# Optimization experiments

Hardware: AMD Instinct MI355X
Metric: run time of the kernel (lower is better)

Reference implementation:

```python
import jax, jax.numpy as jnp
import numpy as np

B, T_IN, D = 8, 512, 384
N_FORMANTS = 1
MAX_DUR = 8               # durations drawn in [0, 8)
T_MEL = T_IN * (MAX_DUR - 1)  # 3584, upper bound on sum of durations
MEL_MAX_LEN = 2048        # static mel_max_len clamp (regulate_len's mel_max_len path)
PACE = 1.0


def setup_inputs() -> dict:
    key = jax.random.key(0)
    k1, k2, k3 = jax.random.split(key, 3)
    enc_out = jax.random.normal(k1, (B, T_IN, D), jnp.float32)
    durations = jax.random.randint(k2, (B, T_IN), 0, MAX_DUR)
    pitch = jax.random.normal(k3, (B, N_FORMANTS, T_MEL), jnp.float32)
    return {"enc_out": enc_out, "durations": durations, "pitch": pitch}


def _regulate_len(durations, enc_out, pace, mel_max_len):
    # reps = round(dur / pace) via floor(x + 0.5), matching torch (reps + 0.5).long()
    reps = jnp.floor(durations.astype(jnp.float32) / pace + 0.5).astype(jnp.int32)  # [B, T_in]
    dec_lens = jnp.minimum(reps.sum(axis=1), mel_max_len)                           # [B]
    # exclusive/inclusive cumsum boundaries, cast to enc dtype as in torch
    cums = jnp.cumsum(jnp.pad(reps, ((0, 0), (1, 0))), axis=1).astype(enc_out.dtype)  # [B, T_in+1]
    rng = jnp.arange(mel_max_len, dtype=enc_out.dtype)[None, :, None]                 # [1, M, 1]
    # one-hot expansion matrix: frame m belongs to token t iff cums[t] <= m < cums[t+1]
    mult = ((cums[:, None, :-1] <= rng) & (cums[:, None, 1:] > rng)).astype(enc_out.dtype)  # [B, M, T_in]
    enc_rep = jnp.einsum('bmt,btd->bmd', mult, enc_out)                               # [B, M, D]
    return enc_rep, dec_lens


def _average_pitch(pitch, durs):
    # pitch: [B, F, T_mel], durs: [B, T_in] (frame counts per token)
    ends = jnp.cumsum(durs, axis=1)                      # [B, T_in] inclusive ends
    starts = jnp.pad(ends[:, :-1], ((0, 0), (1, 0)))     # [B, T_in] exclusive starts
    pc = jnp.pad(jnp.cumsum(pitch, axis=2), ((0, 0), (0, 0), (1, 0)))                         # [B, F, T_mel+1]
    pnz = jnp.pad(jnp.cumsum((pitch != 0.0).astype(pitch.dtype), axis=2), ((0, 0), (0, 0), (1, 0)))
    nf = pitch.shape[1]
    dce = jnp.broadcast_to(ends[:, None, :], (ends.shape[0], nf, ends.shape[1]))
    dcs = jnp.broadcast_to(starts[:, None, :], dce.shape)
    sums = jnp.take_along_axis(pc, dce, axis=2) - jnp.take_along_axis(pc, dcs, axis=2)
    nelems = jnp.take_along_axis(pnz, dce, axis=2) - jnp.take_along_axis(pnz, dcs, axis=2)
    safe = jnp.where(nelems == 0.0, 1.0, nelems)
    return jnp.where(nelems == 0.0, 0.0, sums / safe)   # [B, F, T_in]


def reference(enc_out, durations, pitch):
    enc_rep, dec_lens = _regulate_len(durations, enc_out, PACE, MEL_MAX_LEN)
    pitch_avg = _average_pitch(pitch, durations)
    return enc_rep, dec_lens, pitch_avg
```

## Files before the change

kernel.cpp:

```cpp
#include <hip/hip_runtime.h>

typedef float floatx4 __attribute__((ext_vector_type(4)));

#define NB 8
#define T_IN 512
#define D 384
#define D4 96
#define T_MEL 3584
#define MEL_MAX 2048

#define FRAMES_PER_BLOCK 16
#define GB_PER_BATCH (MEL_MAX / FRAMES_PER_BLOCK)
#define GATHER_BLOCKS (NB * GB_PER_BATCH)
#define PITCH_BLOCKS  (NB * 2)

#define DEC_OFF  ((size_t)NB * MEL_MAX * D)
#define PITCH_OFF (DEC_OFF + NB)

__global__ __launch_bounds__(256) void fp_fused_kernel(
    const int* __restrict__ dur,
    const floatx4* __restrict__ enc4,
    const float* __restrict__ pitch,
    float* __restrict__ out)
{
    const int bid = blockIdx.x;
    const int tid = threadIdx.x;
    const bool isPitch = bid >= GATHER_BLOCKS;
    const int b = isPitch ? ((bid - GATHER_BLOCKS) >> 1) : (bid / GB_PER_BATCH);

    __shared__ int s_ends[T_IN];
    __shared__ int s_wsum[4];
    __shared__ int s_map[FRAMES_PER_BLOCK];

    const int2 dd = ((const int2*)(dur + b * T_IN))[tid];
    int x = dd.x + dd.y;
    #pragma unroll
    for (int off = 1; off < 64; off <<= 1) {
        int y = __shfl_up(x, off, 64);
        if ((tid & 63) >= off) x += y;
    }
    if ((tid & 63) == 63) s_wsum[tid >> 6] = x;
    __syncthreads();
    int woff = 0, total = 0;
    #pragma unroll
    for (int i = 0; i < 4; ++i) {
        int v = s_wsum[i];
        if (i < (tid >> 6)) woff += v;
        total += v;
    }
    const int e1 = woff + x;
    s_ends[2 * tid]     = e1 - dd.y;
    s_ends[2 * tid + 1] = e1;
    __syncthreads();

    if (!isPitch) {
        const int f0 = (bid % GB_PER_BATCH) * FRAMES_PER_BLOCK;
        if (tid < FRAMES_PER_BLOCK) {
            const int f = f0 + tid;
            int tok = -1;
            if (f < total) {
                int lo = 0, hi = T_IN;
                while (lo < hi) {
                    int mid = (lo + hi) >> 1;
                    if (s_ends[mid] > f) hi = mid; else lo = mid + 1;
                }
                tok = lo;
            }
            s_map[tid] = tok;
        }
        if (tid == 0 && bid == b * GB_PER_BATCH)
            out[DEC_OFF + b] = (float)(total < MEL_MAX ? total : MEL_MAX);
        __syncthreads();

        const floatx4* erow = enc4 + (size_t)b * T_IN * D4;
        floatx4* orow = (floatx4*)out + ((size_t)b * MEL_MAX + f0) * D4;
        #pragma unroll
        for (int it = 0; it < (FRAMES_PER_BLOCK * D4) / 256; ++it) {
            const int idx = it * 256 + tid;
            const int fl  = idx / D4;
            const int d4  = idx - fl * D4;
            const int tok = s_map[fl];
            floatx4 v = (floatx4)(0.0f);
            if (tok >= 0) v = erow[(size_t)tok * D4 + d4];
            orow[idx] = v;
        }
    } else {
        const int half = (bid - GATHER_BLOCKS) & 1;
        const int tk = half * 256 + tid;
        const int end   = s_ends[tk];
        const int start = tk ? s_ends[tk - 1] : 0;
        const float* p = pitch + (size_t)b * T_MEL;
        float acc = 0.0f;
        int cnt = 0;
        for (int m = start; m < end; ++m) {
            float v = p[m];
            acc += v;
            cnt += (v != 0.0f) ? 1 : 0;
        }
        out[PITCH_OFF + b * T_IN + tk] = cnt ? acc / (float)cnt : 0.0f;
    }
}

extern "C" void kernel_launch(void* const* d_in, const int* in_sizes, int n_in,
                              void* d_out, int out_size, void* d_ws, size_t ws_size,
                              hipStream_t stream) {
    const float* enc   = (const float*)d_in[0];
    const int*   dur   = (const int*)d_in[1];
    const float* pitch = (const float*)d_in[2];
    float* out = (float*)d_out;

    fp_fused_kernel<<<GATHER_BLOCKS + PITCH_BLOCKS, 256, 0, stream>>>(
        dur, (const floatx4*)enc, pitch, out);
}
```

Measured before the change: 11.83 us.

## Scatter token indices into frame map instead of binary search over shared ends

Drops the shared s_ends array and its extra barrier. Each thread now writes its two tokens' frame ranges directly into the per-block frame-to-token map, replacing a per-frame binary search done by only 16 threads. The pitch path uses one block per batch, with each thread averaging two tokens and storing a float2, and the dec_lens write moves to the pitch blocks. This cuts prologue latency per block, but the scatter loops are serial per thread and the pitch blocks now each do twice the serial work.

```diff
diff --git a/kernel.cpp b/kernel.cpp
--- a/kernel.cpp
+++ b/kernel.cpp
@@ -12,7 +12,7 @@
 #define FRAMES_PER_BLOCK 16
 #define GB_PER_BATCH (MEL_MAX / FRAMES_PER_BLOCK)
 #define GATHER_BLOCKS (NB * GB_PER_BATCH)
-#define PITCH_BLOCKS  (NB * 2)
+#define PITCH_BLOCKS  NB
 
 #define DEC_OFF  ((size_t)NB * MEL_MAX * D)
 #define PITCH_OFF (DEC_OFF + NB)
@@ -26,11 +26,12 @@
     const int bid = blockIdx.x;
     const int tid = threadIdx.x;
     const bool isPitch = bid >= GATHER_BLOCKS;
-    const int b = isPitch ? ((bid - GATHER_BLOCKS) >> 1) : (bid / GB_PER_BATCH);
+    const int b = isPitch ? (bid - GATHER_BLOCKS) : (bid >> 7);
 
-    __shared__ int s_ends[T_IN];
     __shared__ int s_wsum[4];
     __shared__ int s_map[FRAMES_PER_BLOCK];
+
+    if (!isPitch && tid < FRAMES_PER_BLOCK) s_map[tid] = -1;
 
     const int2 dd = ((const int2*)(dur + b * T_IN))[tid];
     int x = dd.x + dd.y;
@@ -48,28 +49,21 @@
         if (i < (tid >> 6)) woff += v;
         total += v;
     }
-    const int e1 = woff + x;
-    s_ends[2 * tid]     = e1 - dd.y;
-    s_ends[2 * tid + 1] = e1;
-    __syncthreads();
+    const int end1   = woff + x;
+    const int start1 = end1 - dd.y;
+    const int start0 = start1 - dd.x;
 
     if (!isPitch) {
-        const int f0 = (bid % GB_PER_BATCH) * FRAMES_PER_BLOCK;
-        if (tid < FRAMES_PER_BLOCK) {
-            const int f = f0 + tid;
-            int tok = -1;
-            if (f < total) {
-                int lo = 0, hi = T_IN;
-                while (lo < hi) {
-                    int mid = (lo + hi) >> 1;
-                    if (s_ends[mid] > f) hi = mid; else lo = mid + 1;
-                }
-                tok = lo;
-            }
-            s_map[tid] = tok;
+        const int f0 = (bid & (GB_PER_BATCH - 1)) * FRAMES_PER_BLOCK;
+        const int f1 = f0 + FRAMES_PER_BLOCK;
+        {
+            const int sA = start0 > f0 ? start0 : f0;
+            const int eA = start1 < f1 ? start1 : f1;
+            for (int f = sA; f < eA; ++f) s_map[f - f0] = 2 * tid;
+            const int sB = start1 > f0 ? start1 : f0;
+            const int eB = end1 < f1 ? end1 : f1;
+            for (int f = sB; f < eB; ++f) s_map[f - f0] = 2 * tid + 1;
         }
-        if (tid == 0 && bid == b * GB_PER_BATCH)
-            out[DEC_OFF + b] = (float)(total < MEL_MAX ? total : MEL_MAX);
         __syncthreads();
 
         const floatx4* erow = enc4 + (size_t)b * T_IN * D4;
@@ -85,19 +79,25 @@
             orow[idx] = v;
         }
     } else {
-        const int half = (bid - GATHER_BLOCKS) & 1;
-        const int tk = half * 256 + tid;
-        const int end   = s_ends[tk];
-        const int start = tk ? s_ends[tk - 1] : 0;
+        if (tid == 0)
+            out[DEC_OFF + b] = (float)(total < MEL_MAX ? total : MEL_MAX);
         const float* p = pitch + (size_t)b * T_MEL;
-        float acc = 0.0f;
-        int cnt = 0;
-        for (int m = start; m < end; ++m) {
-            float v = p[m];
-            acc += v;
-            cnt += (v != 0.0f) ? 1 : 0;
+        float2 r;
+        {
+            float acc = 0.0f; int cnt = 0;
+            for (int m = start0; m < start1; ++m) {
+                float v = p[m]; acc += v; cnt += (v != 0.0f) ? 1 : 0;
+            }
+            r.x = cnt ? acc / (float)cnt : 0.0f;
         }
-        out[PITCH_OFF + b * T_IN + tk] = cnt ? acc / (float)cnt : 0.0f;
+        {
+            float acc = 0.0f; int cnt = 0;
+            for (int m = start1; m < end1; ++m) {
+                float v = p[m]; acc += v; cnt += (v != 0.0f) ? 1 : 0;
+            }
+            r.y = cnt ? acc / (float)cnt : 0.0f;
+        }
+        ((float2*)(out + PITCH_OFF + b * T_IN))[tid] = r;
     }
 }
 
```

Measured after the change: 11.89 us. Within noise of the previous version (+0.5%).
